# Performance work log

Hardware: AMD Instinct MI355X
Metric: run time of the kernel (lower is better)

The kernel has to match this reference:

```python
import jax, jax.numpy as jnp
import numpy as np

N = 80000
E = 1280000
EPS = 1e-5

def _lrelu(x):
    return jax.nn.leaky_relu(x, 0.01)

def _bn(h):
    # training-mode BatchNorm1d with batch size 1: stats over the node dim; affine is identity at init
    return (h - h.mean(0)) / jnp.sqrt(h.var(0) + EPS)

def _ln(h, g, b):
    m = h.mean(-1, keepdims=True)
    v = h.var(-1, keepdims=True)
    return (h - m) / jnp.sqrt(v + EPS) * g + b

def _gcn(h, w, b, src, dst, n):
    # PyG GCNConv: add self loops, symmetric deg^-1/2 normalization, aggregate at target
    hw = h @ w.T
    loop = jnp.arange(n, dtype=src.dtype)
    s = jnp.concatenate([src, loop])
    d = jnp.concatenate([dst, loop])
    deg = jax.ops.segment_sum(jnp.ones(d.shape, hw.dtype), d, num_segments=n)
    dinv = jnp.where(deg > 0, 1.0 / jnp.sqrt(deg), 0.0)
    msg = hw[s] * (dinv[s] * dinv[d])[:, None]  # [E+N, C]
    return jax.ops.segment_sum(msg, d, num_segments=n) + b

def _tnet(x, c1w, c1b, c2w, c2b, c3w, c3b, f1w, f1b, f2w, f2b, f3w, f3b):
    h = jax.nn.relu(x @ c1w.T + c1b)          # [N,64]  (source skips bn1)
    h = jax.nn.relu(_bn(h @ c2w.T + c2b))     # [N,128]
    h = jax.nn.relu(_bn(h @ c3w.T + c3b))     # [N,1024]
    g = h.max(0)                              # global max pool -> [1024]
    g = jax.nn.relu(g @ f1w.T + f1b)
    g = jax.nn.relu(g @ f2w.T + f2b)
    iden = jnp.array([1.0, 0.0, 0.0, 0.0, 1.0, 0.0, 0.0, 0.0, 1.0], x.dtype)
    g = g @ f3w.T + f3b + iden
    return g.reshape(3, 3)

def _forward(edge_index, x, tnet_c1_w, tnet_c1_b, tnet_c2_w, tnet_c2_b, tnet_c3_w, tnet_c3_b, tnet_fc1_w, tnet_fc1_b, tnet_fc2_w, tnet_fc2_b, tnet_fc3_w, tnet_fc3_b, conv1_w, conv1_b, g1_li_w, g1_li_b, g1_gcn_w, g1_gcn_b, g1_ln_g, g1_ln_b, conv2_w, conv2_b, g2_li_w, g2_li_b, g2_gcn_w, g2_gcn_b, g2_ln_g, g2_ln_b, conv3_w, conv3_b, out_w, out_b):
    src, dst = edge_index[0], edge_index[1]
    n = x.shape[0]
    T = _tnet(x, tnet_c1_w, tnet_c1_b, tnet_c2_w, tnet_c2_b, tnet_c3_w, tnet_c3_b, tnet_fc1_w, tnet_fc1_b, tnet_fc2_w, tnet_fc2_b, tnet_fc3_w, tnet_fc3_b)
    h0 = x @ T                                  # [N,3] spatial transform
    xg = _lrelu(h0 @ conv1_w.T + conv1_b)       # [N,64] (conv1d k=1 == per-node linear)
    # Gcn_Attention 1
    nf = _lrelu(xg @ g1_li_w.T + g1_li_b)
    nf2 = _lrelu(_gcn(nf, g1_gcn_w, g1_gcn_b, src, dst, n))
    h = _ln(jnp.concatenate([nf, nf2], 1), g1_ln_g, g1_ln_b)   # [N,128]
    h = _lrelu(h @ conv2_w.T + conv2_b)
    # Gcn_Attention 2
    nf = _lrelu(h @ g2_li_w.T + g2_li_b)
    nf2 = _lrelu(_gcn(nf, g2_gcn_w, g2_gcn_b, src, dst, n))
    h = _ln(jnp.concatenate([nf, nf2], 1), g2_ln_g, g2_ln_b)   # [N,256]
    h = jnp.concatenate([h, xg], 1)                            # [N,320]
    h = _lrelu(h @ conv3_w.T + conv3_b)                        # [N,256]
    pooled = h.mean(0)                                         # global mean pool (single graph)
    feat = jnp.concatenate([jnp.broadcast_to(pooled, (n, pooled.shape[0])), xg], 1)  # [N,320]
    return feat @ out_w.T + out_b                              # [N,4]

def setup_inputs():
    ki = iter(jax.random.split(jax.random.key(0), 32))
    def W(shape):
        return jax.random.normal(next(ki), shape, jnp.float32) * (1.0 / float(np.sqrt(shape[-1])))
    z = lambda n: jnp.zeros((n,), jnp.float32)
    o = lambda n: jnp.ones((n,), jnp.float32)
    inp = {}
    inp['x'] = jax.random.normal(next(ki), (N, 3), jnp.float32)
    inp['edge_index'] = jax.random.randint(next(ki), (2, E), 0, N, dtype=jnp.int32)
    inp['tnet_c1_w'] = W((64, 3)); inp['tnet_c1_b'] = z(64)
    inp['tnet_c2_w'] = W((128, 64)); inp['tnet_c2_b'] = z(128)
    inp['tnet_c3_w'] = W((1024, 128)); inp['tnet_c3_b'] = z(1024)
    inp['tnet_fc1_w'] = W((512, 1024)); inp['tnet_fc1_b'] = z(512)
    inp['tnet_fc2_w'] = W((256, 512)); inp['tnet_fc2_b'] = z(256)
    inp['tnet_fc3_w'] = W((9, 256)); inp['tnet_fc3_b'] = z(9)
    inp['conv1_w'] = W((64, 3)); inp['conv1_b'] = z(64)
    inp['g1_li_w'] = W((64, 64)); inp['g1_li_b'] = z(64)
    inp['g1_gcn_w'] = W((64, 64)); inp['g1_gcn_b'] = z(64)
    inp['g1_ln_g'] = o(128); inp['g1_ln_b'] = z(128)
    inp['conv2_w'] = W((128, 128)); inp['conv2_b'] = z(128)
    inp['g2_li_w'] = W((128, 128)); inp['g2_li_b'] = z(128)
    inp['g2_gcn_w'] = W((128, 128)); inp['g2_gcn_b'] = z(128)
    inp['g2_ln_g'] = o(256); inp['g2_ln_b'] = z(256)
    inp['conv3_w'] = W((256, 320)); inp['conv3_b'] = z(256)
    inp['out_w'] = W((4, 320)); inp['out_b'] = z(4)
    return inp

def reference(x, edge_index, tnet_c1_w, tnet_c1_b, tnet_c2_w, tnet_c2_b, tnet_c3_w, tnet_c3_b, tnet_fc1_w, tnet_fc1_b, tnet_fc2_w, tnet_fc2_b, tnet_fc3_w, tnet_fc3_b, conv1_w, conv1_b, g1_li_w, g1_li_b, g1_gcn_w, g1_gcn_b, g1_ln_g, g1_ln_b, conv2_w, conv2_b, g2_li_w, g2_li_b, g2_gcn_w, g2_gcn_b, g2_ln_g, g2_ln_b, conv3_w, conv3_b, out_w, out_b):
    return _forward(edge_index, x, tnet_c1_w, tnet_c1_b, tnet_c2_w, tnet_c2_b, tnet_c3_w, tnet_c3_b, tnet_fc1_w, tnet_fc1_b, tnet_fc2_w, tnet_fc2_b, tnet_fc3_w, tnet_fc3_b, conv1_w, conv1_b, g1_li_w, g1_li_b, g1_gcn_w, g1_gcn_b, g1_ln_g, g1_ln_b, conv2_w, conv2_b, g2_li_w, g2_li_b, g2_gcn_w, g2_gcn_b, g2_ln_g, g2_ln_b, conv3_w, conv3_b, out_w, out_b)
```

## Files before the change

### kernel.cpp

```cpp
#include <hip/hip_runtime.h>
#include <cstddef>

#define EPSV 1e-5f

typedef __attribute__((ext_vector_type(8))) short frag8;
typedef __attribute__((ext_vector_type(4))) float f32x4;

__device__ __forceinline__ float lrelu01(float v) { return v > 0.f ? v : 0.01f * v; }
__device__ __forceinline__ void atomAddF(float* p, float v) { unsafeAtomicAdd(p, v); }
__device__ __forceinline__ unsigned fkey(float f) {
    unsigned u = __float_as_uint(f);
    return (u & 0x80000000u) ? ~u : (u | 0x80000000u);
}
__device__ __forceinline__ unsigned short f2b(float f) {
    unsigned u = __float_as_uint(f);
    unsigned r = u + 0x7fffu + ((u >> 16) & 1u);
    return (unsigned short)(r >> 16);
}
__device__ __forceinline__ float b2f(unsigned short h) {
    return __uint_as_float(((unsigned)h) << 16);
}
__device__ __forceinline__ float blo(unsigned u) { return __uint_as_float(u << 16); }
__device__ __forceinline__ float bhi(unsigned u) { return __uint_as_float(u & 0xffff0000u); }

static inline unsigned cdivu(unsigned a, unsigned b) { return (a + b - 1) / b; }


__device__ void degrank_body(int bid, const int* __restrict__ dst, int* __restrict__ deg,
                             int* __restrict__ rank, int E) {
    int e = bid * 256 + threadIdx.x;
    if (e < E) rank[e] = atomicAdd(&deg[dst[e]], 1);
}

__device__ void scan_local_body(int bid, const int* __restrict__ deg, int* __restrict__ startv,
                                int* __restrict__ bsum, float* __restrict__ dinv, int n) {
    __shared__ int t0[256];
    int tid = threadIdx.x;
    int i = bid * 256 + tid;
    int v = (i < n) ? deg[i] : 0;
    if (i < n) dinv[i] = rsqrtf((float)(v + 1));
    t0[tid] = v;
    __syncthreads();
    for (int o = 1; o < 256; o <<= 1) {
        int add = (tid >= o) ? t0[tid - o] : 0;
        __syncthreads();
        t0[tid] += add;
        __syncthreads();
    }
    if (i < n) startv[i] = t0[tid] - v;
    if (tid == 255) bsum[bid] = t0[255];
}

__device__ void scan_bsum_body(int* __restrict__ bsum, int nb) {
    __shared__ int t0[512];
    __shared__ int t1[512];
    int tid = threadIdx.x;
    int v0 = (tid < nb) ? bsum[tid] : 0;
    int v1 = (tid + 256 < nb) ? bsum[tid + 256] : 0;
    t0[tid] = v0; t0[tid + 256] = v1;
    __syncthreads();
    int* a = t0; int* b = t1;
    for (int o = 1; o < 512; o <<= 1) {
        b[tid]       = a[tid]       + ((tid >= o)       ? a[tid - o]       : 0);
        b[tid + 256] = a[tid + 256] + ((tid + 256 >= o) ? a[tid + 256 - o] : 0);
        __syncthreads();
        int* t = a; a = b; b = t;
    }
    if (tid < nb) bsum[tid] = a[tid] - v0;
    if (tid + 256 < nb) bsum[tid + 256] = a[tid + 256] - v1;
}

__device__ void scan_add_body(int bid, int* __restrict__ startv, const int* __restrict__ bsum, int n) {
    int i = bid * 256 + threadIdx.x;
    if (i < n) startv[i] += bsum[bid];
}

__device__ void fill_body(int bid, const int* __restrict__ src, const int* __restrict__ dst,
                          const int* __restrict__ rank, const int* __restrict__ startv,
                          int* __restrict__ csr, int E) {
    int e = bid * 256 + threadIdx.x;
    if (e < E) csr[startv[dst[e]] + rank[e]] = src[e];
}


__device__ void wconv_body(int bid, const float* __restrict__ s0, const float* __restrict__ s1,
                           const float* __restrict__ s2, const float* __restrict__ s3,
                           const float* __restrict__ s4, const float* __restrict__ s5,
                           const float* __restrict__ s6, const float* __restrict__ s7,
                           unsigned short* __restrict__ dst) {
    int t = bid * 256 + threadIdx.x;
    if (t >= 278528) return;
    const float* srcs[8] = {s0, s1, s2, s3, s4, s5, s6, s7};
    const int off[9] = {0, 8192, 139264, 143360, 147456, 163840, 180224, 196608, 278528};
    int seg = 0;
    while (t >= off[seg + 1]) ++seg;
    unsigned short v = f2b(srcs[seg][t - off[seg]]);
    if (seg == 1) {
        int li = t - 8192;
        int rch = li >> 7, k = li & 127;
        int cb = rch >> 7, r = rch & 127;
        int flat = ((r >> 4) * 4 + (k >> 5)) * 64 + ((k >> 3) & 3) * 16 + (r & 15);
        dst[8192 + cb * 16384 + flat * 8 + (k & 7)] = v;
    } else {
        dst[t] = v;
    }
}

__device__ void h1_body(int bid, const float* __restrict__ x, const float* __restrict__ w,
                        const float* __restrict__ b, unsigned short* __restrict__ h1, int n) {
    int node = bid * 256 + threadIdx.x;
    if (node >= n) return;
    float x0 = x[node * 3], x1 = x[node * 3 + 1], x2 = x[node * 3 + 2];
    unsigned short* o = h1 + (size_t)node * 64;
#pragma unroll
    for (int cp = 0; cp < 8; ++cp) {
        unsigned short tmp[8];
#pragma unroll
        for (int t = 0; t < 8; ++t) {
            int c = cp * 8 + t;
            float v = x0 * w[c * 3] + x1 * w[c * 3 + 1] + x2 * w[c * 3 + 2] + b[c];
            tmp[t] = f2b(fmaxf(v, 0.f));
        }
        *(float4*)(o + cp * 8) = *(float4*)tmp;
    }
}

__device__ void prebn_body(int bid, const float* __restrict__ z, const float* __restrict__ sum2,
                           const float* __restrict__ ss2, unsigned short* __restrict__ a3f,
                           int n16, float invn) {
    int t = bid * 256 + threadIdx.x;
    if (t >= n16) return;
    int row = t >> 4, cp = t & 15;
    int c = cp * 8;
    const float* src = z + (size_t)row * 128 + c;
    float4 v0 = *(const float4*)src;
    float4 v1 = *(const float4*)(src + 4);
    float vv[8] = {v0.x, v0.y, v0.z, v0.w, v1.x, v1.y, v1.z, v1.w};
    unsigned short o[8];
#pragma unroll
    for (int i = 0; i < 8; ++i) {
        float m = sum2[c + i] * invn;
        float var = ss2[c + i] * invn - m * m;
        o[i] = f2b(fmaxf((vv[i] - m) * rsqrtf(var + EPSV), 0.f));
    }
    int tile = row >> 7, r = row & 127;
    int flat = ((r >> 4) * 4 + (cp >> 2)) * 64 + (cp & 3) * 16 + (r & 15);
    *(float4*)(a3f + (size_t)tile * 16384 + flat * 8) = *(float4*)o;
}

__device__ void head_body(const float* __restrict__ sum3, const float* __restrict__ ss3,
                          const unsigned* __restrict__ maxk,
                          const float* __restrict__ f1w, const float* __restrict__ f1b,
                          const float* __restrict__ f2w, const float* __restrict__ f2b,
                          const float* __restrict__ f3w, const float* __restrict__ f3b,
                          float* __restrict__ T9, float invn) {
    __shared__ float g[1024];
    __shared__ float a1[512];
    __shared__ float a2[256];
    int tid = threadIdx.x;
    for (int c = tid; c < 1024; c += 256) {
        float m = sum3[c] * invn;
        float var = ss3[c] * invn - m * m;
        unsigned k = maxk[c];
        unsigned u = (k & 0x80000000u) ? (k & 0x7FFFFFFFu) : ~k;
        g[c] = fmaxf((__uint_as_float(u) - m) * rsqrtf(var + EPSV), 0.f);
    }
    __syncthreads();
#pragma unroll
    for (int h = 0; h < 2; ++h) {
        int r = tid + h * 256;
        const float* w = f1w + (size_t)r * 1024;
        float sp[4];
#pragma unroll
        for (int part = 0; part < 4; ++part) {
            float s = 0.f;
            const float* wp = w + part * 256;
            const float* gp = g + part * 256;
            for (int k = 0; k < 256; ++k) s = fmaf(wp[k], gp[k], s);
            sp[part] = s;
        }
        a1[r] = fmaxf(((sp[0] + sp[1]) + (sp[2] + sp[3])) + f1b[r], 0.f);
    }
    __syncthreads();
    {
        const float* w = f2w + (size_t)tid * 512;
        float s = f2b[tid];
        for (int k = 0; k < 512; ++k) s = fmaf(w[k], a1[k], s);
        a2[tid] = fmaxf(s, 0.f);
    }
    __syncthreads();
    if (tid < 9) {
        const float* w = f3w + (size_t)tid * 256;
        float s = f3b[tid];
        for (int k = 0; k < 256; ++k) s = fmaf(w[k], a2[k], s);
        if (tid == 0 || tid == 4 || tid == 8) s += 1.f;
        T9[tid] = s;
    }
}

enum { MF_BIAS = 1, MF_LRELU = 2, MF_DINV = 4, MF_STOREF = 8, MF_STOREB = 16,
       MF_STATS = 32, MF_COLSUM = 64 };

template <int BN, int MODE>
__device__ void mgemm_body(int bx, int by,
                           const unsigned short* __restrict__ A, int lda, int K,
                           const unsigned short* __restrict__ W,
                           const float* __restrict__ bias,
                           float* __restrict__ OutF, unsigned short* __restrict__ OutB, int ldo,
                           const float* __restrict__ dinv,
                           float* __restrict__ sum_o, float* __restrict__ ss_o,
                           unsigned* __restrict__ maxk_o) {
    constexpr int BM = 128;
    constexpr int LDT = 40;
    __shared__ unsigned short As[BM * LDT];
    __shared__ unsigned short Ws[BN * LDT];
    __shared__ float redS[2 * 128];
    __shared__ unsigned redM[128];

    const int tid = threadIdx.x;
    const int wid = tid >> 6, lane = tid & 63;
    const int quad = lane >> 4, lrow = lane & 15;
    const int bn0 = bx * BM;
    const int bc0 = by * BN;

    constexpr int NI = (BN == 128) ? 4 : 2;
    constexpr int NJ = 4;
    const int wm = (BN == 128) ? (wid & 1) * 64 : wid * 32;
    const int wn = (BN == 128) ? (wid >> 1) * 64 : 0;

    if (MODE & (MF_STATS | MF_COLSUM)) {
        for (int c = tid; c < BN; c += 256) {
            redS[c] = 0.f; redS[128 + c] = 0.f; redM[c] = 0u;
        }
    }

    f32x4 acc[NI][NJ] = {};

    for (int k0 = 0; k0 < K; k0 += 32) {
#pragma unroll
        for (int h = 0; h < 2; ++h) {
            int ch = tid + h * 256;
            int row = ch >> 2, cp = ch & 3;
            const unsigned short* src = A + (size_t)(bn0 + row) * lda + k0 + cp * 8;
            *(float4*)&As[row * LDT + cp * 8] = *(const float4*)src;
        }
#pragma unroll
        for (int h = 0; h < BN / 64; ++h) {
            int ch = tid + h * 256;
            int row = ch >> 2, cp = ch & 3;
            const unsigned short* src = W + (size_t)(bc0 + row) * K + k0 + cp * 8;
            *(float4*)&Ws[row * LDT + cp * 8] = *(const float4*)src;
        }
        __syncthreads();
        frag8 af[NI], bf[NJ];
#pragma unroll
        for (int i = 0; i < NI; ++i)
            af[i] = *(const frag8*)&As[(wm + i * 16 + lrow) * LDT + quad * 8];
#pragma unroll
        for (int j = 0; j < NJ; ++j)
            bf[j] = *(const frag8*)&Ws[(wn + j * 16 + lrow) * LDT + quad * 8];
#pragma unroll
        for (int i = 0; i < NI; ++i)
#pragma unroll
            for (int j = 0; j < NJ; ++j)
                acc[i][j] = __builtin_amdgcn_mfma_f32_16x16x32_bf16(af[i], bf[j], acc[i][j], 0, 0, 0);
        __syncthreads();
    }

#pragma unroll
    for (int j = 0; j < NJ; ++j) {
        const int col = bc0 + wn + j * 16 + lrow;
        float bv = (MODE & MF_BIAS) ? bias[col] : 0.f;
        float s = 0.f, q = 0.f, m = -3.4e38f;
#pragma unroll
        for (int i = 0; i < NI; ++i) {
            const int rowb = bn0 + wm + i * 16 + quad * 4;
#pragma unroll
            for (int r = 0; r < 4; ++r) {
                float t = acc[i][j][r] + bv;
                if (MODE & MF_LRELU) t = lrelu01(t);
                if (MODE & MF_DINV) t *= dinv[rowb + r];
                if (MODE & MF_STOREF) OutF[(size_t)(rowb + r) * ldo + col] = t;
                if (MODE & MF_STOREB) OutB[(size_t)(rowb + r) * ldo + col] = f2b(t);
                s += t; q += t * t; m = fmaxf(m, t);
            }
        }
        if (MODE & (MF_STATS | MF_COLSUM)) {
            s += __shfl_xor(s, 16); s += __shfl_xor(s, 32);
            if (MODE & MF_STATS) {
                q += __shfl_xor(q, 16); q += __shfl_xor(q, 32);
                m = fmaxf(m, __shfl_xor(m, 16)); m = fmaxf(m, __shfl_xor(m, 32));
            }
            if (quad == 0) {
                int lc = wn + j * 16 + lrow;
                atomicAdd(&redS[lc], s);
                if (MODE & MF_STATS) {
                    atomicAdd(&redS[128 + lc], q);
                    atomicMax(&redM[lc], fkey(m));
                }
            }
        }
    }
    if (MODE & (MF_STATS | MF_COLSUM)) {
        __syncthreads();
        for (int c = tid; c < BN; c += 256) {
            atomAddF(&sum_o[bc0 + c], redS[c]);
            if (MODE & MF_STATS) {
                atomAddF(&ss_o[bc0 + c], redS[128 + c]);
                atomicMax(&maxk_o[bc0 + c], redM[c]);
            }
        }
    }
}

template <int BN, int MODE, int SWAP>
__launch_bounds__(256)
__global__ void k_mgemm(const unsigned short* __restrict__ A, int lda, int K,
                        const unsigned short* __restrict__ W,
                        const float* __restrict__ bias,
                        float* __restrict__ OutF, unsigned short* __restrict__ OutB, int ldo,
                        const float* __restrict__ dinv,
                        float* __restrict__ sum_o, float* __restrict__ ss_o,
                        unsigned* __restrict__ maxk_o) {
    int bx = SWAP ? blockIdx.y : blockIdx.x;
    int by = SWAP ? blockIdx.x : blockIdx.y;
    mgemm_body<BN, MODE>(bx, by, A, lda, K, W, bias, OutF, OutB, ldo, dinv, sum_o, ss_o, maxk_o);
}

__device__ void z3_body(int bid,
                        const unsigned short* __restrict__ AF,
                        const unsigned short* __restrict__ WF,
                        const float* __restrict__ bias,
                        float* __restrict__ sum_o, float* __restrict__ ss_o,
                        unsigned* __restrict__ maxk_o, int ntiles) {
    const int tid = threadIdx.x;
    const int wid = tid >> 6, lane = tid & 63;
    const int quad = lane >> 4, lrow = lane & 15;

    int w = (bid & 7) * ntiles + (bid >> 3);
    const int tile = w >> 3;
    const int cb = w & 7;
    const unsigned short* At = AF + (size_t)tile * 16384;
    const unsigned short* Wt = WF + (size_t)cb * 16384;

    const int ar = (wid & 1) * 4;
    const int wc = (wid >> 1) * 4;
    f32x4 acc[4][4] = {};
#pragma unroll
    for (int kc = 0; kc < 4; ++kc) {
        frag8 af[4], bf[4];
#pragma unroll
        for (int i = 0; i < 4; ++i)
            af[i] = *(const frag8*)&At[(((ar + i) * 4 + kc) * 64 + lane) * 8];
#pragma unroll
        for (int j = 0; j < 4; ++j)
            bf[j] = *(const frag8*)&Wt[(((wc + j) * 4 + kc) * 64 + lane) * 8];
#pragma unroll
        for (int i = 0; i < 4; ++i)
#pragma unroll
            for (int j = 0; j < 4; ++j)
                acc[i][j] = __builtin_amdgcn_mfma_f32_16x16x32_bf16(af[i], bf[j], acc[i][j], 0, 0, 0);
    }

#pragma unroll
    for (int j = 0; j < 4; ++j) {
        int c = cb * 128 + (wc + j) * 16 + lrow;
        float bv = bias[c];
        float s = 0.f, q = 0.f, m = -3.4e38f;
#pragma unroll
        for (int i = 0; i < 4; ++i)
#pragma unroll
            for (int r = 0; r < 4; ++r) {
                float t = acc[i][j][r] + bv;
                s += t; q += t * t; m = fmaxf(m, t);
            }
        s += __shfl_xor(s, 16); s += __shfl_xor(s, 32);
        q += __shfl_xor(q, 16); q += __shfl_xor(q, 32);
        m = fmaxf(m, __shfl_xor(m, 16)); m = fmaxf(m, __shfl_xor(m, 32));
        if (quad == 0) {
            atomAddF(&sum_o[c], s);
            atomAddF(&ss_o[c], q);
            atomicMax(&maxk_o[c], fkey(m));
        }
    }
}


__launch_bounds__(256)
__global__ void FK1(const int* __restrict__ dst, int* __restrict__ deg, int* __restrict__ rank,
                    int E, int EB,
                    const float* s0, const float* s1, const float* s2, const float* s3,
                    const float* s4, const float* s5, const float* s6, const float* s7,
                    unsigned short* __restrict__ WB, int WCB,
                    const float* __restrict__ x, const float* __restrict__ c1w,
                    const float* __restrict__ c1b, unsigned short* __restrict__ B1, int n) {
    int b = blockIdx.x;
    if (b < EB) { degrank_body(b, dst, deg, rank, E); return; }
    b -= EB;
    if (b < WCB) { wconv_body(b, s0, s1, s2, s3, s4, s5, s6, s7, WB); return; }
    b -= WCB;
    h1_body(b, x, c1w, c1b, B1, n);
}

__launch_bounds__(256)
__global__ void FK2(const unsigned short* __restrict__ A, int lda, int K,
                    const unsigned short* __restrict__ W, const float* __restrict__ bias,
                    float* __restrict__ OutF, int ldo,
                    float* __restrict__ sum_o, float* __restrict__ ss_o,
                    unsigned* __restrict__ maxk_o, int GXz,
                    const int* __restrict__ deg, int* __restrict__ startv,
                    int* __restrict__ bsum, float* __restrict__ dinvv, int n) {
    if ((int)blockIdx.x < GXz)
        mgemm_body<128, (MF_BIAS | MF_STOREF | MF_STATS)>(
            blockIdx.x, 0, A, lda, K, W, bias, OutF, nullptr, ldo, nullptr, sum_o, ss_o, maxk_o);
    else
        scan_local_body(blockIdx.x - GXz, deg, startv, bsum, dinvv, n);
}

__launch_bounds__(256)
__global__ void FK3(const float* __restrict__ z, const float* __restrict__ sum2,
                    const float* __restrict__ ss2, unsigned short* __restrict__ a3f,
                    int n16, float invn, int PB, int* __restrict__ bsum, int nb) {
    if ((int)blockIdx.x < PB) prebn_body(blockIdx.x, z, sum2, ss2, a3f, n16, invn);
    else scan_bsum_body(bsum, nb);
}

__launch_bounds__(256)
__global__ void FK4(const unsigned short* __restrict__ AF, const unsigned short* __restrict__ WF,
                    const float* __restrict__ bias,
                    float* __restrict__ sum_o, float* __restrict__ ss_o,
                    unsigned* __restrict__ maxk_o, int ntiles, int NZ,
                    int* __restrict__ startv, const int* __restrict__ bsum, int n) {
    if ((int)blockIdx.x < NZ) z3_body(blockIdx.x, AF, WF, bias, sum_o, ss_o, maxk_o, ntiles);
    else scan_add_body(blockIdx.x - NZ, startv, bsum, n);
}

__launch_bounds__(256)
__global__ void FK5(const int* __restrict__ src, const int* __restrict__ dst,
                    const int* __restrict__ rank, const int* __restrict__ startv,
                    int* __restrict__ csr, int E, int EB,
                    const float* __restrict__ sum3, const float* __restrict__ ss3,
                    const unsigned* __restrict__ maxk,
                    const float* __restrict__ f1w, const float* __restrict__ f1b,
                    const float* __restrict__ f2w, const float* __restrict__ f2b,
                    const float* __restrict__ f3w, const float* __restrict__ f3b,
                    float* __restrict__ T9, float invn) {
    if ((int)blockIdx.x < EB) fill_body(blockIdx.x, src, dst, rank, startv, csr, E);
    else head_body(sum3, ss3, maxk, f1w, f1b, f2w, f2b, f3w, f3b, T9, invn);
}

template <int CH>
__launch_bounds__(256)
__global__ void k_gln(const int* __restrict__ startv, const int* __restrict__ degv,
                      const int* __restrict__ csr, const unsigned short* __restrict__ q,
                      const unsigned short* __restrict__ nf, const float* __restrict__ dinv,
                      const float* __restrict__ gcn_b, const float* __restrict__ lng,
                      const float* __restrict__ lnb, unsigned short* __restrict__ outp,
                      int ldo, int n) {
    constexpr int GRP = (CH == 64) ? 8 : 4;
    constexpr int PL  = 64 / GRP;
    constexpr int TT  = 16 / GRP;
    constexpr int CPL = CH / PL;
    const int wv = threadIdx.x >> 6, lane = threadIdx.x & 63;
    const int g = lane / PL, p = lane & (PL - 1);
    int node = blockIdx.x * 4 + wv;
    if (node >= n) return;

    const unsigned short* qp = q + (size_t)p * CPL;

    float acc[CPL];
    {
        uint4 v = *(const uint4*)(qp + (size_t)node * CH);
        unsigned sv[4] = {v.x, v.y, v.z, v.w};
        if (g == 0) {
#pragma unroll
            for (int d = 0; d < 4; ++d) { acc[2 * d] = blo(sv[d]); acc[2 * d + 1] = bhi(sv[d]); }
        } else {
#pragma unroll
            for (int k = 0; k < CPL; ++k) acc[k] = 0.f;
        }
    }

    int s0 = startv[node], cnt = degv[node];
    const int* cs = csr + s0;
    int sidx[TT];
#pragma unroll
    for (int t = 0; t < TT; ++t) { int j = t * GRP + g; sidx[t] = (j < cnt) ? cs[j] : n; }
    for (int j0 = 0; j0 < cnt; j0 += 16) {
        uint4 buf[TT];
#pragma unroll
        for (int t = 0; t < TT; ++t)
            buf[t] = *(const uint4*)(qp + (size_t)(unsigned)sidx[t] * CH);
#pragma unroll
        for (int t = 0; t < TT; ++t) {
            int j = j0 + 16 + t * GRP + g;
            sidx[t] = (j < cnt) ? cs[j] : n;
        }
#pragma unroll
        for (int t = 0; t < TT; ++t) {
            unsigned bw[4] = {buf[t].x, buf[t].y, buf[t].z, buf[t].w};
#pragma unroll
            for (int d = 0; d < 4; ++d) {
                acc[2 * d] += blo(bw[d]);
                acc[2 * d + 1] += bhi(bw[d]);
            }
        }
    }

#pragma unroll
    for (int k = 0; k < CPL; ++k) {
#pragma unroll
        for (int off = PL; off < 64; off <<= 1) acc[k] += __shfl_xor(acc[k], off);
    }

    float di = dinv[node];
    float nv[CPL], bv[CPL];
    {
        uint4 v = *(const uint4*)(nf + (size_t)node * CH + p * CPL);
        unsigned sv[4] = {v.x, v.y, v.z, v.w};
#pragma unroll
        for (int d = 0; d < 4; ++d) { nv[2 * d] = blo(sv[d]); nv[2 * d + 1] = bhi(sv[d]); }
    }
    const float* gb = gcn_b + p * CPL;
#pragma unroll
    for (int k = 0; k < CPL; ++k) bv[k] = lrelu01(di * acc[k] + gb[k]);

    float s = 0.f, ss = 0.f;
#pragma unroll
    for (int k = 0; k < CPL; ++k) { s += nv[k] + bv[k]; ss += nv[k] * nv[k] + bv[k] * bv[k]; }
#pragma unroll
    for (int off = 32; off > 0; off >>= 1) { s += __shfl_xor(s, off); ss += __shfl_xor(ss, off); }
    const float inv = 1.f / (float)(GRP * 2 * CH);
    float mu = s * inv;
    float var = ss * inv - mu * mu;
    float rsg = rsqrtf(var + EPSV);

    unsigned short* orow = outp + (size_t)node * ldo;
    if (g == 0) {
        unsigned short tmp[CPL];
        const float* lg = lng + p * CPL; const float* lb = lnb + p * CPL;
#pragma unroll
        for (int k = 0; k < CPL; ++k) tmp[k] = f2b((nv[k] - mu) * rsg * lg[k] + lb[k]);
        *(uint4*)(orow + p * CPL) = *(uint4*)tmp;
    } else if (g == 1) {
        unsigned short tmp[CPL];
        const float* lg = lng + CH + p * CPL; const float* lb = lnb + CH + p * CPL;
#pragma unroll
        for (int k = 0; k < CPL; ++k) tmp[k] = f2b((bv[k] - mu) * rsg * lg[k] + lb[k]);
        *(uint4*)(orow + CH + p * CPL) = *(uint4*)tmp;
    }
}


__global__ void k_xg(const float* __restrict__ x, const float* __restrict__ T9,
                     const float* __restrict__ w, const float* __restrict__ b,
                     unsigned short* __restrict__ xg, int n) {
    int node = blockIdx.x * 256 + threadIdx.x;
    if (node >= n) return;
    float x0 = x[node * 3], x1 = x[node * 3 + 1], x2 = x[node * 3 + 2];
    float h0 = x0 * T9[0] + x1 * T9[3] + x2 * T9[6];
    float h1 = x0 * T9[1] + x1 * T9[4] + x2 * T9[7];
    float h2 = x0 * T9[2] + x1 * T9[5] + x2 * T9[8];
    unsigned short* o = xg + (size_t)node * 320;
#pragma unroll
    for (int cp = 0; cp < 8; ++cp) {
        unsigned short tmp[8];
#pragma unroll
        for (int t = 0; t < 8; ++t) {
            int c = cp * 8 + t;
            float v = h0 * w[c * 3] + h1 * w[c * 3 + 1] + h2 * w[c * 3 + 2] + b[c];
            tmp[t] = f2b(lrelu01(v));
        }
        *(float4*)(o + cp * 8) = *(float4*)tmp;
    }
}

template <int BN>
__launch_bounds__(256)
__global__ void k_ligc(const unsigned short* __restrict__ A, int lda, int K,
                       const unsigned short* __restrict__ Wli, const float* __restrict__ bli,
                       const unsigned short* __restrict__ Wgc, const float* __restrict__ dinv,
                       unsigned short* __restrict__ NF, int ldnf,
                       unsigned short* __restrict__ Q, int ldq) {
    constexpr int BM = 128;
    constexpr int LDT = 40;
    constexpr int LDT2 = BN + 8;
    __shared__ unsigned short SA[BM * LDT2];
    __shared__ unsigned short Ws[BN * LDT];

    const int tid = threadIdx.x;
    const int wid = tid >> 6, lane = tid & 63;
    const int quad = lane >> 4, lrow = lane & 15;
    const int bn0 = blockIdx.x * BM;
    constexpr int NI = (BN == 128) ? 4 : 2;
    constexpr int NJ = 4;
    const int wm = (BN == 128) ? (wid & 1) * 64 : wid * 32;
    const int wn = (BN == 128) ? (wid >> 1) * 64 : 0;

    {
        f32x4 acc[NI][NJ] = {};
        for (int k0 = 0; k0 < K; k0 += 32) {
#pragma unroll
            for (int h = 0; h < 2; ++h) {
                int ch = tid + h * 256;
                int row = ch >> 2, cp = ch & 3;
                *(float4*)&SA[row * LDT + cp * 8] =
                    *(const float4*)(A + (size_t)(bn0 + row) * lda + k0 + cp * 8);
            }
#pragma unroll
            for (int h = 0; h < BN / 64; ++h) {
                int ch = tid + h * 256;
                int row = ch >> 2, cp = ch & 3;
                *(float4*)&Ws[row * LDT + cp * 8] =
                    *(const float4*)(Wli + (size_t)row * K + k0 + cp * 8);
            }
            __syncthreads();
            frag8 af[NI], bf[NJ];
#pragma unroll
            for (int i = 0; i < NI; ++i)
                af[i] = *(const frag8*)&SA[(wm + i * 16 + lrow) * LDT + quad * 8];
#pragma unroll
            for (int j = 0; j < NJ; ++j)
                bf[j] = *(const frag8*)&Ws[(wn + j * 16 + lrow) * LDT + quad * 8];
#pragma unroll
            for (int i = 0; i < NI; ++i)
#pragma unroll
                for (int j = 0; j < NJ; ++j)
                    acc[i][j] = __builtin_amdgcn_mfma_f32_16x16x32_bf16(af[i], bf[j], acc[i][j], 0, 0, 0);
            __syncthreads();
        }
#pragma unroll
        for (int j = 0; j < NJ; ++j) {
            const int col = wn + j * 16 + lrow;
            float bv = bli[col];
#pragma unroll
            for (int i = 0; i < NI; ++i) {
                const int rowl = wm + i * 16 + quad * 4;
#pragma unroll
                for (int r = 0; r < 4; ++r) {
                    unsigned short h = f2b(lrelu01(acc[i][j][r] + bv));
                    NF[(size_t)(bn0 + rowl + r) * ldnf + col] = h;
                    SA[(rowl + r) * LDT2 + col] = h;
                }
            }
        }
        __syncthreads();
    }
    {
        f32x4 acc[NI][NJ] = {};
        for (int k0 = 0; k0 < BN; k0 += 32) {
#pragma unroll
            for (int h = 0; h < BN / 64; ++h) {
                int ch = tid + h * 256;
                int row = ch >> 2, cp = ch & 3;
                *(float4*)&Ws[row * LDT + cp * 8] =
                    *(const float4*)(Wgc + (size_t)row * BN + k0 + cp * 8);
            }
            __syncthreads();
            frag8 af[NI], bf[NJ];
#pragma unroll
            for (int i = 0; i < NI; ++i)
                af[i] = *(const frag8*)&SA[(wm + i * 16 + lrow) * LDT2 + k0 + quad * 8];
#pragma unroll
            for (int j = 0; j < NJ; ++j)
                bf[j] = *(const frag8*)&Ws[(wn + j * 16 + lrow) * LDT + quad * 8];
#pragma unroll
            for (int i = 0; i < NI; ++i)
#pragma unroll
                for (int j = 0; j < NJ; ++j)
                    acc[i][j] = __builtin_amdgcn_mfma_f32_16x16x32_bf16(af[i], bf[j], acc[i][j], 0, 0, 0);
            __syncthreads();
        }
#pragma unroll
        for (int j = 0; j < NJ; ++j) {
            const int col = wn + j * 16 + lrow;
#pragma unroll
            for (int i = 0; i < NI; ++i) {
                const int rowb = bn0 + wm + i * 16 + quad * 4;
#pragma unroll
                for (int r = 0; r < 4; ++r) {
                    float t = acc[i][j][r] * dinv[rowb + r];
                    Q[(size_t)(rowb + r) * ldq + col] = f2b(t);
                }
            }
        }
    }
}

__global__ void k_out2(const unsigned short* __restrict__ hcat, const float* __restrict__ ow,
                       const float* __restrict__ ob, const float* __restrict__ pooled,
                       float* __restrict__ out, int n, float invn) {
    __shared__ float c4s[4];
    int tid = threadIdx.x;
    {
        int j = tid >> 6, lane = tid & 63;
        float s = 0.f;
        for (int c = lane; c < 256; c += 64) s += pooled[c] * invn * ow[j * 320 + c];
#pragma unroll
        for (int off = 32; off > 0; off >>= 1) s += __shfl_down(s, off);
        if (lane == 0) c4s[j] = s + ob[j];
    }
    __syncthreads();
    int node = blockIdx.x * 256 + tid;
    if (node >= n) return;
    const unsigned short* xgp = hcat + (size_t)node * 320 + 256;
    float s0 = c4s[0], s1 = c4s[1], s2 = c4s[2], s3 = c4s[3];
#pragma unroll
    for (int cp = 0; cp < 8; ++cp) {
        float4 raw = *(const float4*)(xgp + cp * 8);
        unsigned short tmp[8];
        *(float4*)tmp = raw;
#pragma unroll
        for (int t = 0; t < 8; ++t) {
            int k = 256 + cp * 8 + t;
            float f = b2f(tmp[t]);
            s0 = fmaf(f, ow[k], s0);
            s1 = fmaf(f, ow[320 + k], s1);
            s2 = fmaf(f, ow[640 + k], s2);
            s3 = fmaf(f, ow[960 + k], s3);
        }
    }
    *(float4*)(out + (size_t)node * 4) = make_float4(s0, s1, s2, s3);
}


extern "C" void kernel_launch(void* const* d_in, const int* in_sizes, int n_in,
                              void* d_out, int out_size, void* d_ws, size_t ws_size,
                              hipStream_t stream) {
    const float* x   = (const float*)d_in[0];
    const int*   ei  = (const int*)d_in[1];
    const float* c1w = (const float*)d_in[2];  const float* c1b = (const float*)d_in[3];
    const float* c2w = (const float*)d_in[4];  const float* c2b = (const float*)d_in[5];
    const float* c3w = (const float*)d_in[6];  const float* c3b = (const float*)d_in[7];
    const float* f1w = (const float*)d_in[8];  const float* f1b = (const float*)d_in[9];
    const float* f2w = (const float*)d_in[10]; const float* f2b = (const float*)d_in[11];
    const float* f3w = (const float*)d_in[12]; const float* f3b = (const float*)d_in[13];
    const float* cv1w = (const float*)d_in[14]; const float* cv1b = (const float*)d_in[15];
    const float* li1w = (const float*)d_in[16]; const float* li1b = (const float*)d_in[17];
    const float* gc1w = (const float*)d_in[18]; const float* gc1b = (const float*)d_in[19];
    const float* ln1g = (const float*)d_in[20]; const float* ln1b = (const float*)d_in[21];
    const float* cv2w = (const float*)d_in[22]; const float* cv2b = (const float*)d_in[23];
    const float* li2w = (const float*)d_in[24]; const float* li2b = (const float*)d_in[25];
    const float* gc2w = (const float*)d_in[26]; const float* gc2b = (const float*)d_in[27];
    const float* ln2g = (const float*)d_in[28]; const float* ln2b = (const float*)d_in[29];
    const float* cv3w = (const float*)d_in[30]; const float* cv3b = (const float*)d_in[31];
    const float* ow  = (const float*)d_in[32]; const float* ob  = (const float*)d_in[33];
    float* out = (float*)d_out;

    const int N = in_sizes[0] / 3;
    const int E = in_sizes[1] / 2;
    const int* srcI = ei;
    const int* dstI = ei + E;

    char* base = (char*)d_ws;
    size_t off = 0;
    auto take = [&](size_t bytes) -> char* {
        char* p = base + off;
        off = (off + bytes + 255) & ~(size_t)255;
        return p;
    };
    int*   deg    = (int*)  take((size_t)N * 4);
    float* dinv   = (float*)take((size_t)N * 4);
    int*   startv = (int*)  take((size_t)N * 4);
    int*   rank   = (int*)  take((size_t)E * 4);
    int*   csr    = (int*)  take((size_t)E * 4);
    int*   bsum   = (int*)  take(512 * 4);
    float* sm     = (float*)take(8192 * 4);
    unsigned short* WB = (unsigned short*)take(278528 * 2);
    unsigned short* H  = (unsigned short*)take((size_t)N * 320 * 2);
    float* F1 = (float*)take((size_t)N * 128 * 4);
    unsigned short* B1 = (unsigned short*)take((size_t)N * 64 * 2);
    unsigned short* B2 = (unsigned short*)take(((size_t)N * 128 + 128) * 2);
    unsigned short* B3 = (unsigned short*)take((size_t)N * 128 * 2);

    unsigned short* c2wb  = WB + 0;
    unsigned short* c3wf  = WB + 8192;
    unsigned short* li1wb = WB + 139264;
    unsigned short* gc1wb = WB + 143360;
    unsigned short* cv2wb = WB + 147456;
    unsigned short* li2wb = WB + 163840;
    unsigned short* gc2wb = WB + 180224;
    unsigned short* cv3wb = WB + 196608;

    float* sum2 = sm + 0;    float* ss2 = sm + 128;
    float* sum3 = sm + 256;  float* ss3 = sm + 1280;
    unsigned* maxk = (unsigned*)(sm + 2304);
    float* pooled = sm + 3328;
    unsigned* dmax = (unsigned*)(sm + 3584);
    float* T9  = sm + 3968;

    const float invn = 1.0f / (float)N;
    const dim3 blk(256);
    const unsigned GX = (unsigned)(N / 128);
    const unsigned NB = cdivu((unsigned)N, 256);
    const unsigned EB = cdivu((unsigned)E, 256);
    const unsigned WCB = cdivu(278528u, 256);
    const unsigned PB = cdivu((unsigned)N * 16, 256);

    hipMemsetAsync(deg, 0, (size_t)N * 4, stream);
    hipMemsetAsync(sm, 0, 3712 * 4, stream);
    hipMemsetAsync(B2 + (size_t)N * 128, 0, 256, stream);

    FK1<<<EB + WCB + NB, blk, 0, stream>>>(dstI, deg, rank, E, (int)EB,
                                           c2w, c3w, li1w, gc1w, cv2w, li2w, gc2w, cv3w,
                                           WB, (int)WCB, x, c1w, c1b, B1, N);
    FK2<<<GX + NB, blk, 0, stream>>>(B1, 64, 64, c2wb, c2b, F1, 128,
                                     sum2, ss2, dmax, (int)GX, deg, startv, bsum, dinv, N);
    FK3<<<PB + 1, blk, 0, stream>>>(F1, sum2, ss2, B2, N * 16, invn, (int)PB, bsum, (int)NB);
    FK4<<<8 * GX + NB, blk, 0, stream>>>(B2, c3wf, c3b, sum3, ss3, maxk, (int)GX,
                                         (int)(8 * GX), startv, bsum, N);
    hipMemsetAsync(B2 + (size_t)N * 64, 0, 128, stream);
    FK5<<<EB + 1, blk, 0, stream>>>(srcI, dstI, rank, startv, csr, E, (int)EB,
                                    sum3, ss3, maxk, f1w, f1b, f2w, f2b, f3w, f3b, T9, invn);

    k_xg<<<NB, blk, 0, stream>>>(x, T9, cv1w, cv1b, H + 256, N);

    k_ligc<64><<<GX, blk, 0, stream>>>(H + 256, 320, 64, li1wb, li1b, gc1wb, dinv, B1, 64, B2, 64);
    k_gln<64><<<cdivu((unsigned)N, 4), blk, 0, stream>>>(
        startv, deg, csr, B2, B1, dinv, gc1b, ln1g, ln1b, B3, 128, N);
    k_mgemm<128, (MF_BIAS | MF_LRELU | MF_STOREB), 0><<<dim3(GX, 1), blk, 0, stream>>>(
        B3, 128, 128, cv2wb, cv2b, nullptr, B2, 128, nullptr, nullptr, nullptr, nullptr);

    k_ligc<128><<<GX, blk, 0, stream>>>(B2, 128, 128, li2wb, li2b, gc2wb, dinv, B3, 128, B2, 128);
    k_gln<128><<<cdivu((unsigned)N, 4), blk, 0, stream>>>(
        startv, deg, csr, B2, B3, dinv, gc2b, ln2g, ln2b, H, 320, N);

    k_mgemm<128, (MF_BIAS | MF_LRELU | MF_COLSUM), 1><<<dim3(2, GX), blk, 0, stream>>>(
        H, 320, 320, cv3wb, cv3b, nullptr, nullptr, 0, nullptr, pooled, nullptr, nullptr);

    k_out2<<<NB, blk, 0, stream>>>(H, ow, ob, pooled, out, N, invn);
}
```

Baseline: 587.5 us.

## Parallelize TNet FC head across blocks and fold fc3 into xg kernel

Replaces the single-block serial FC head (fc1/fc2/fc3 done by one workgroup) with fc1 split across 8 blocks using shuffle-reduced partial dot products, a separate 8-block fc2 kernel, and fc3 recomputed per block inside the xg transform kernel. This targets a long serial tail where one block performed about 700K FMAs while the rest of the GPU sat idle. It adds one extra kernel launch and redundant fc3 work in every xg block. Fc1 blocks are placed first in FK5 so they are scheduled early.

```diff
diff --git a/kernel.cpp b/kernel.cpp
--- a/kernel.cpp
+++ b/kernel.cpp
@@ -148,15 +148,11 @@
     *(float4*)(a3f + (size_t)tile * 16384 + flat * 8) = *(float4*)o;
 }
 
-__device__ void head_body(const float* __restrict__ sum3, const float* __restrict__ ss3,
-                          const unsigned* __restrict__ maxk,
-                          const float* __restrict__ f1w, const float* __restrict__ f1b,
-                          const float* __restrict__ f2w, const float* __restrict__ f2b,
-                          const float* __restrict__ f3w, const float* __restrict__ f3b,
-                          float* __restrict__ T9, float invn) {
+__device__ void fc1_body(int bid, const float* __restrict__ sum3, const float* __restrict__ ss3,
+                         const unsigned* __restrict__ maxk,
+                         const float* __restrict__ f1w, const float* __restrict__ f1b,
+                         float* __restrict__ a1, float invn) {
     __shared__ float g[1024];
-    __shared__ float a1[512];
-    __shared__ float a2[256];
     int tid = threadIdx.x;
     for (int c = tid; c < 1024; c += 256) {
         float m = sum3[c] * invn;
@@ -166,36 +162,21 @@
         g[c] = fmaxf((__uint_as_float(u) - m) * rsqrtf(var + EPSV), 0.f);
     }
     __syncthreads();
-#pragma unroll
-    for (int h = 0; h < 2; ++h) {
-        int r = tid + h * 256;
-        const float* w = f1w + (size_t)r * 1024;
-        float sp[4];
-#pragma unroll
-        for (int part = 0; part < 4; ++part) {
-            float s = 0.f;
-            const float* wp = w + part * 256;
-            const float* gp = g + part * 256;
-            for (int k = 0; k < 256; ++k) s = fmaf(wp[k], gp[k], s);
-            sp[part] = s;
-        }
-        a1[r] = fmaxf(((sp[0] + sp[1]) + (sp[2] + sp[3])) + f1b[r], 0.f);
-    }
-    __syncthreads();
-    {
-        const float* w = f2w + (size_t)tid * 512;
-        float s = f2b[tid];
-        for (int k = 0; k < 512; ++k) s = fmaf(w[k], a1[k], s);
-        a2[tid] = fmaxf(s, 0.f);
-    }
-    __syncthreads();
-    if (tid < 9) {
-        const float* w = f3w + (size_t)tid * 256;
-        float s = f3b[tid];
-        for (int k = 0; k < 256; ++k) s = fmaf(w[k], a2[k], s);
-        if (tid == 0 || tid == 4 || tid == 8) s += 1.f;
-        T9[tid] = s;
-    }
+    int row = bid * 64 + (tid >> 2);
+    int part = tid & 3;
+    const float* w = f1w + (size_t)row * 1024 + part * 256;
+    const float* gg = g + part * 256;
+    float s = 0.f;
+#pragma unroll 4
+    for (int k = 0; k < 256; k += 4) {
+        float4 wv = *(const float4*)(w + k);
+        s = fmaf(wv.x, gg[k], s);
+        s = fmaf(wv.y, gg[k + 1], s);
+        s = fmaf(wv.z, gg[k + 2], s);
+        s = fmaf(wv.w, gg[k + 3], s);
+    }
+    s += __shfl_xor(s, 1); s += __shfl_xor(s, 2);
+    if (part == 0) a1[row] = fmaxf(s + f1b[row], 0.f);
 }
 
 enum { MF_BIAS = 1, MF_LRELU = 2, MF_DINV = 4, MF_STOREF = 8, MF_STOREB = 16,
@@ -438,15 +419,39 @@
 __launch_bounds__(256)
 __global__ void FK5(const int* __restrict__ src, const int* __restrict__ dst,
                     const int* __restrict__ rank, const int* __restrict__ startv,
-                    int* __restrict__ csr, int E, int EB,
+                    int* __restrict__ csr, int E,
                     const float* __restrict__ sum3, const float* __restrict__ ss3,
                     const unsigned* __restrict__ maxk,
                     const float* __restrict__ f1w, const float* __restrict__ f1b,
-                    const float* __restrict__ f2w, const float* __restrict__ f2b,
-                    const float* __restrict__ f3w, const float* __restrict__ f3b,
-                    float* __restrict__ T9, float invn) {
-    if ((int)blockIdx.x < EB) fill_body(blockIdx.x, src, dst, rank, startv, csr, E);
-    else head_body(sum3, ss3, maxk, f1w, f1b, f2w, f2b, f3w, f3b, T9, invn);
+                    float* __restrict__ a1, float invn) {
+    int b = blockIdx.x;
+    if (b < 8) { fc1_body(b, sum3, ss3, maxk, f1w, f1b, a1, invn); return; }
+    fill_body(b - 8, src, dst, rank, startv, csr, E);
+}
+
+__launch_bounds__(256)
+__global__ void k_fc2(const float* __restrict__ a1, const float* __restrict__ f2w,
+                      const float* __restrict__ f2bias, float* __restrict__ a2) {
+    __shared__ float a1s[512];
+    int tid = threadIdx.x;
+    a1s[tid] = a1[tid];
+    a1s[tid + 256] = a1[tid + 256];
+    __syncthreads();
+    int row = blockIdx.x * 32 + (tid >> 3);
+    int part = tid & 7;
+    const float* w = f2w + (size_t)row * 512 + part * 64;
+    const float* aa = a1s + part * 64;
+    float s = 0.f;
+#pragma unroll 4
+    for (int k = 0; k < 64; k += 4) {
+        float4 wv = *(const float4*)(w + k);
+        s = fmaf(wv.x, aa[k], s);
+        s = fmaf(wv.y, aa[k + 1], s);
+        s = fmaf(wv.z, aa[k + 2], s);
+        s = fmaf(wv.w, aa[k + 3], s);
+    }
+    s += __shfl_xor(s, 1); s += __shfl_xor(s, 2); s += __shfl_xor(s, 4);
+    if (part == 0) a2[row] = fmaxf(s + f2bias[row], 0.f);
 }
 
 template <int CH>
@@ -552,15 +557,38 @@
 }
 
 
-__global__ void k_xg(const float* __restrict__ x, const float* __restrict__ T9,
-                     const float* __restrict__ w, const float* __restrict__ b,
-                     unsigned short* __restrict__ xg, int n) {
-    int node = blockIdx.x * 256 + threadIdx.x;
+__launch_bounds__(256)
+__global__ void k_xg2(const float* __restrict__ x, const float* __restrict__ a2,
+                      const float* __restrict__ f3w, const float* __restrict__ f3b,
+                      const float* __restrict__ w, const float* __restrict__ b,
+                      unsigned short* __restrict__ xg, int n) {
+    __shared__ float a2s[256];
+    __shared__ float T9s[9];
+    int tid = threadIdx.x;
+    a2s[tid] = a2[tid];
+    __syncthreads();
+    if (tid < 144) {
+        int r = tid >> 4, kk = (tid & 15) * 16;
+        const float* wr = f3w + r * 256 + kk;
+        const float* ar = a2s + kk;
+        float s = 0.f;
+#pragma unroll
+        for (int k = 0; k < 16; ++k) s = fmaf(wr[k], ar[k], s);
+        s += __shfl_xor(s, 1); s += __shfl_xor(s, 2);
+        s += __shfl_xor(s, 4); s += __shfl_xor(s, 8);
+        if ((tid & 15) == 0) {
+            s += f3b[r];
+            if (r == 0 || r == 4 || r == 8) s += 1.f;
+            T9s[r] = s;
+        }
+    }
+    __syncthreads();
+    int node = blockIdx.x * 256 + tid;
     if (node >= n) return;
     float x0 = x[node * 3], x1 = x[node * 3 + 1], x2 = x[node * 3 + 2];
-    float h0 = x0 * T9[0] + x1 * T9[3] + x2 * T9[6];
-    float h1 = x0 * T9[1] + x1 * T9[4] + x2 * T9[7];
-    float h2 = x0 * T9[2] + x1 * T9[5] + x2 * T9[8];
+    float h0 = x0 * T9s[0] + x1 * T9s[3] + x2 * T9s[6];
+    float h1 = x0 * T9s[1] + x1 * T9s[4] + x2 * T9s[7];
+    float h2 = x0 * T9s[2] + x1 * T9s[5] + x2 * T9s[8];
     unsigned short* o = xg + (size_t)node * 320;
 #pragma unroll
     for (int cp = 0; cp < 8; ++cp) {
@@ -733,7 +761,7 @@
     const float* c2w = (const float*)d_in[4];  const float* c2b = (const float*)d_in[5];
     const float* c3w = (const float*)d_in[6];  const float* c3b = (const float*)d_in[7];
     const float* f1w = (const float*)d_in[8];  const float* f1b = (const float*)d_in[9];
-    const float* f2w = (const float*)d_in[10]; const float* f2b = (const float*)d_in[11];
+    const float* f2w = (const float*)d_in[10]; const float* f2bp = (const float*)d_in[11];
     const float* f3w = (const float*)d_in[12]; const float* f3b = (const float*)d_in[13];
     const float* cv1w = (const float*)d_in[14]; const float* cv1b = (const float*)d_in[15];
     const float* li1w = (const float*)d_in[16]; const float* li1b = (const float*)d_in[17];
@@ -787,7 +815,8 @@
     unsigned* maxk = (unsigned*)(sm + 2304);
     float* pooled = sm + 3328;
     unsigned* dmax = (unsigned*)(sm + 3584);
-    float* T9  = sm + 3968;
+    float* a1  = sm + 5120;
+    float* a2  = sm + 5760;
 
     const float invn = 1.0f / (float)N;
     const dim3 blk(256);
@@ -810,10 +839,10 @@
     FK4<<<8 * GX + NB, blk, 0, stream>>>(B2, c3wf, c3b, sum3, ss3, maxk, (int)GX,
                                          (int)(8 * GX), startv, bsum, N);
     hipMemsetAsync(B2 + (size_t)N * 64, 0, 128, stream);
-    FK5<<<EB + 1, blk, 0, stream>>>(srcI, dstI, rank, startv, csr, E, (int)EB,
-                                    sum3, ss3, maxk, f1w, f1b, f2w, f2b, f3w, f3b, T9, invn);
-
-    k_xg<<<NB, blk, 0, stream>>>(x, T9, cv1w, cv1b, H + 256, N);
+    FK5<<<8 + EB, blk, 0, stream>>>(srcI, dstI, rank, startv, csr, E,
+                                    sum3, ss3, maxk, f1w, f1b, a1, invn);
+    k_fc2<<<8, blk, 0, stream>>>(a1, f2w, f2bp, a2);
+    k_xg2<<<NB, blk, 0, stream>>>(x, a2, f3w, f3b, cv1w, cv1b, H + 256, N);
 
     k_ligc<64><<<GX, blk, 0, stream>>>(H + 256, 320, 64, li1wb, li1b, gc1wb, dinv, B1, 64, B2, 64);
     k_gln<64><<<cdivu((unsigned)N, 4), blk, 0, stream>>>(
```

After: 506.7 us. 1.16x faster.
